# Kernel optimization log

Measured on AMD Instinct MI355X. Metric: run time of the kernel, lower is better.

The kernel has to match this reference:

```python
import jax, jax.numpy as jnp
import numpy as np

V, E, H, T = 50000, 1024, 1024, 128
L, MAXL = 50, 50
PAD, O_TOK = 0, 1


def setup_inputs() -> dict:
    key = jax.random.key(0)
    ks = jax.random.split(key, 18)
    s = 0.05
    f = lambda k, shape: jax.random.normal(k, shape, jnp.float32) * s
    return {
        'input_ids': jax.random.randint(ks[0], (1, L), 1, V),
        'tag_ids': jax.random.randint(ks[1], (1, L), 1, T),  # >=1 so no pad tags
        'word_embed': f(ks[2], (V, E)),
        'enc_Wih': f(ks[3], (3 * H, E)),
        'enc_Whh': f(ks[4], (3 * H, H)),
        'enc_bih': f(ks[5], (3 * H,)),
        'enc_bhh': f(ks[6], (3 * H,)),
        'dec_embed': f(ks[7], (T, H)),
        'attn_W': f(ks[8], (MAXL, 2 * H)),
        'attn_b': f(ks[9], (MAXL,)),
        'comb_W': f(ks[10], (H, 2 * H)),
        'comb_b': f(ks[11], (H,)),
        'dec_Wih': f(ks[12], (3 * H, H)),
        'dec_Whh': f(ks[13], (3 * H, H)),
        'dec_bih': f(ks[14], (3 * H,)),
        'dec_bhh': f(ks[15], (3 * H,)),
        'out_W': f(ks[16], (T, H)),
        'out_b': f(ks[17], (T,)),
    }


def _gru_cell(x, h, Wih, Whh, bih, bhh):
    # PyTorch GRU cell semantics
    gi = Wih @ x + bih
    gh = Whh @ h + bhh
    i_r, i_z, i_n = jnp.split(gi, 3)
    h_r, h_z, h_n = jnp.split(gh, 3)
    r = jax.nn.sigmoid(i_r + h_r)
    z = jax.nn.sigmoid(i_z + h_z)
    n = jnp.tanh(i_n + r * h_n)
    return (1.0 - z) * n + z * h


def _forward(word_embed, enc_Wih, enc_Whh, enc_bih, enc_bhh,
             dec_embed, attn_W, attn_b, comb_W, comb_b,
             dec_Wih, dec_Whh, dec_bih, dec_bhh, out_W, out_b,
             input_ids, tag_ids):
    src = input_ids[0]  # (L,)
    tgt = tag_ids[0]    # (L,)

    def enc_step(h, tok):
        h2 = _gru_cell(word_embed[tok], h, enc_Wih, enc_Whh, enc_bih, enc_bhh)
        return h2, h2

    h_enc, enc_outs = jax.lax.scan(enc_step, jnp.zeros((H,), word_embed.dtype), src)
    # enc_outs: (L, H); L == MAX_LENGTH so the buffer is fully filled

    dec_in = jnp.concatenate([jnp.array([O_TOK], tgt.dtype), tgt[:-1]])  # teacher forcing

    def dec_step(h, xt):
        tok, tgt_t = xt
        e = dec_embed[tok]  # (H,), dropout is identity in eval
        aw = jax.nn.softmax(attn_W @ jnp.concatenate([e, h]) + attn_b)  # (MAXL,)
        ctx = aw @ enc_outs  # (H,)
        o = jax.nn.relu(comb_W @ jnp.concatenate([e, ctx]) + comb_b)
        h2 = _gru_cell(o, h, dec_Wih, dec_Whh, dec_bih, dec_bhh)
        logp = jax.nn.log_softmax(out_W @ h2 + out_b)  # decoder output (log-probs)
        # original applies CrossEntropyLoss on log-probs -> log_softmax applied twice
        nll = -jax.nn.log_softmax(logp)[tgt_t]
        step_loss = jnp.where(tgt_t == PAD, jnp.zeros((), logp.dtype), nll)
        return h2, (logp, step_loss)

    _, (logps, losses) = jax.lax.scan(dec_step, h_enc, (dec_in, tgt))
    return logps, jnp.sum(losses)  # (L, T), scalar


def reference(input_ids, tag_ids, word_embed, enc_Wih, enc_Whh, enc_bih, enc_bhh,
              dec_embed, attn_W, attn_b, comb_W, comb_b,
              dec_Wih, dec_Whh, dec_bih, dec_bhh, out_W, out_b):
    return _forward(word_embed, enc_Wih, enc_Whh, enc_bih, enc_bhh,
                    dec_embed, attn_W, attn_b, comb_W, comb_b,
                    dec_Wih, dec_Whh, dec_bih, dec_bhh, out_W, out_b,
                    input_ids, tag_ids)
```

## Files before the change

### kernel.cpp

```cpp
#include <hip/hip_runtime.h>
#include <cstdint>


#define HDIM 1024
#define LSEQ 50
#define TDIM 128
#define G3   3072
#define PB   6
#define NPROD 128
#define LSTR 68

typedef float f32x4 __attribute__((ext_vector_type(4)));

struct KArgs {
  const int* input_ids; const int* tag_ids;
  const float* word_embed;
  const float* enc_Wih; const float* enc_Whh; const float* enc_bih; const float* enc_bhh;
  const float* dec_embed; const float* attn_W; const float* attn_b;
  const float* comb_W; const float* comb_b;
  const float* dec_Wih; const float* dec_Whh; const float* dec_bih; const float* dec_bhh;
  const float* out_W; const float* out_b;
  float* out;
  unsigned* ctrP; unsigned* ctrE; unsigned* ctrM; unsigned* ctrO; unsigned* ctrV;
  float* hbE;
  float* hbD;
  float* obD;
  float* awb;
  float* logits;
  float* GI;
  float* attn_e;
  float* pre_comb;
  float* MT;
  float* enc_outs;
};

__device__ __forceinline__ void fence_vm(){
  asm volatile("s_waitcnt vmcnt(0)" ::: "memory");
}
__device__ __forceinline__ void st_coh(float* p, float v){
  __hip_atomic_store(p, v, __ATOMIC_RELAXED, __HIP_MEMORY_SCOPE_AGENT);
}
__device__ __forceinline__ void st_tag(float* p, float v, unsigned tag){
  unsigned b = (__float_as_uint(v) & ~31u) | tag;
  st_coh(p, __uint_as_float(b));
}
__device__ __forceinline__ void stf(unsigned* p, unsigned v){
  __hip_atomic_store(p, v, __ATOMIC_RELAXED, __HIP_MEMORY_SCOPE_AGENT);
}
__device__ __forceinline__ unsigned ldu(const unsigned* p){
  return __hip_atomic_load(p, __ATOMIC_RELAXED, __HIP_MEMORY_SCOPE_AGENT);
}
__device__ __forceinline__ void addc(unsigned* base, int bid){
  __hip_atomic_fetch_add(base + (bid&7)*16, 1u, __ATOMIC_RELAXED, __HIP_MEMORY_SCOPE_AGENT);
}
__device__ __forceinline__ void addc0(unsigned* base){
  __hip_atomic_fetch_add(base, 1u, __ATOMIC_RELAXED, __HIP_MEMORY_SCOPE_AGENT);
}
__device__ __forceinline__ f32x4 coh_load4(const float* p){
  f32x4 v;
  asm volatile("global_load_dwordx4 %0, %1, off sc0 sc1\n\ts_waitcnt vmcnt(0)"
               : "=v"(v) : "v"(p) : "memory");
  return v;
}

template<int N>
__device__ __forceinline__ void wred_batch(float* v){
  #pragma unroll
  for(int o=32;o>0;o>>=1){
    #pragma unroll
    for(int i=0;i<N;i++) v[i] += __shfl_xor(v[i],o,64);
  }
}
__device__ __forceinline__ float wred_sum(float v){
  #pragma unroll
  for(int o=32;o>0;o>>=1) v += __shfl_xor(v,o,64);
  return v;
}
__device__ __forceinline__ float wred_max(float v){
  #pragma unroll
  for(int o=32;o>0;o>>=1) v = fmaxf(v,__shfl_xor(v,o,64));
  return v;
}

struct Chunk { f32x4 a,b,c,d; };
__device__ __forceinline__ Chunk load_chunk(const float* __restrict__ row, int lane){
  const f32x4* p = reinterpret_cast<const f32x4*>(row) + lane*4;
  Chunk w; w.a=p[0]; w.b=p[1]; w.c=p[2]; w.d=p[3]; return w;
}
__device__ __forceinline__ void pin(Chunk& c){
  asm volatile("" : "+v"(c.a), "+v"(c.b), "+v"(c.c), "+v"(c.d));
}
__device__ __forceinline__ void pinf(float& x){
  asm volatile("" : "+v"(x));
}
__device__ __forceinline__ float chunk_dot(const Chunk& w, const float* hc){
  return w.a.x*hc[0]+w.a.y*hc[1]+w.a.z*hc[2]+w.a.w*hc[3]
       + w.b.x*hc[4]+w.b.y*hc[5]+w.b.z*hc[6]+w.b.w*hc[7]
       + w.c.x*hc[8]+w.c.y*hc[9]+w.c.z*hc[10]+w.c.w*hc[11]
       + w.d.x*hc[12]+w.d.y*hc[13]+w.d.z*hc[14]+w.d.w*hc[15];
}
__device__ __forceinline__ void load_vec16(const float* __restrict__ v, float* hc, int lane){
  const f32x4* p = reinterpret_cast<const f32x4*>(v) + lane*4;
  f32x4 x0=p[0],x1=p[1],x2=p[2],x3=p[3];
  hc[0]=x0.x; hc[1]=x0.y; hc[2]=x0.z; hc[3]=x0.w;
  hc[4]=x1.x; hc[5]=x1.y; hc[6]=x1.z; hc[7]=x1.w;
  hc[8]=x2.x; hc[9]=x2.y; hc[10]=x2.z; hc[11]=x2.w;
  hc[12]=x3.x; hc[13]=x3.y; hc[14]=x3.z; hc[15]=x3.w;
}
__device__ __forceinline__ float sigm(float x){ return 1.f/(1.f+expf(-x)); }

template<int SLP>
__device__ __forceinline__ void stage_tag(float* ldsb, const float* g, int tid, unsigned tag){
  const float* p = g + 4*tid;
  f32x4 v;
  for(;;){
    v = coh_load4(p);
    unsigned m = ((__float_as_uint(v.x)&31u)^tag) | ((__float_as_uint(v.y)&31u)^tag)
               | ((__float_as_uint(v.z)&31u)^tag) | ((__float_as_uint(v.w)&31u)^tag);
    if(m==0u) break;
    if(SLP) __builtin_amdgcn_s_sleep(SLP);
  }
  int q = tid>>2, r4 = (tid&3)*4;
  ldsb[(r4+0)*LSTR+q]=v.x; ldsb[(r4+1)*LSTR+q]=v.y;
  ldsb[(r4+2)*LSTR+q]=v.z; ldsb[(r4+3)*LSTR+q]=v.w;
}
__device__ __forceinline__ void read16(const float* ldsb, float* hc, int lane){
  #pragma unroll
  for(int k=0;k<16;k++) hc[k]=ldsb[k*LSTR+lane];
}

__device__ __forceinline__ void wait8(const unsigned* base, unsigned n, int lane){
  const unsigned* p = base + lane*16;
  for(;;){
    unsigned v = (lane<8)? ldu(p) : 0xFFFFFFFFu;
    if(__all((int)(v>=n))) return;
    __builtin_amdgcn_s_sleep(8);
  }
}

__global__ __launch_bounds__(256,1) void seq2seq_kernel(KArgs A){
  const int bid = blockIdx.x, tid = threadIdx.x;
  const int wave = tid>>6, lane = tid&63;
  __shared__ float lds_h[16*LSTR+16];
  __shared__ float lds_o[16*LSTR+16];
  __shared__ float smr[64];
  __shared__ float smL[TDIM];
  __shared__ float smA[64];

  const int gv = bid*4 + wave;

  {
    const int r0 = gv*3;
    Chunk w0 = load_chunk(A.enc_Wih + (size_t)r0*HDIM, lane);
    Chunk w1 = load_chunk(A.enc_Wih + (size_t)(r0+1)*HDIM, lane);
    Chunk w2 = load_chunk(A.enc_Wih + (size_t)(r0+2)*HDIM, lane);
    float b0=A.enc_bih[r0], b1=A.enc_bih[r0+1], b2=A.enc_bih[r0+2];
    for(int te=0;te<LSEQ;++te){
      int tok = A.input_ids[te];
      float ec[16]; load_vec16(A.word_embed + (size_t)tok*HDIM, ec, lane);
      float d[3];
      d[0]=chunk_dot(w0,ec); d[1]=chunk_dot(w1,ec); d[2]=chunk_dot(w2,ec);
      wred_batch<3>(d);
      if(lane==0){
        st_coh(&A.GI[te*G3+r0],   d[0]+b0);
        st_coh(&A.GI[te*G3+r0+1], d[1]+b1);
        st_coh(&A.GI[te*G3+r0+2], d[2]+b2);
      }
    }
    Chunk wc = load_chunk(A.comb_W + (size_t)gv*2*HDIM, lane);
    float bc = A.comb_b[gv];
    Chunk wa; wa.a=0.f; wa.b=0.f; wa.c=0.f; wa.d=0.f;
    float ba = 0.f;
    if(gv < LSEQ){ wa = load_chunk(A.attn_W + (size_t)gv*2*HDIM, lane); ba = A.attn_b[gv]; }
    for(int t=0;t<LSEQ;++t){
      int tok = (t==0)?1:A.tag_ids[t-1];
      float ec[16]; load_vec16(A.dec_embed + (size_t)tok*HDIM, ec, lane);
      float d[2];
      d[0]=chunk_dot(wc,ec);
      d[1]=(gv<LSEQ)? chunk_dot(wa,ec) : 0.f;
      wred_batch<2>(d);
      if(lane==0){
        st_coh(&A.pre_comb[t*HDIM+gv], d[0]+bc);
        if(gv<LSEQ) st_coh(&A.attn_e[t*LSEQ+gv], d[1]+ba);
      }
    }
  }
  fence_vm();
  __syncthreads();
  if(tid==0) addc(A.ctrP, bid);
  if(wave==0) wait8(A.ctrP, 32u, lane);
  __syncthreads();

  const int p = bid - PB;
  const bool is_prod = (p>=0 && p<NPROD);
  const int base = is_prod ? p*8 : 0;
  const int j8 = base + (tid&7);

  if(is_prod){
    Chunk we[6];
    #pragma unroll
    for(int i=0;i<6;i++){
      int r = wave + 4*i;
      int le=r/3, g=r-3*le, row=g*HDIM+base+le;
      we[i] = load_chunk(A.enc_Whh + (size_t)row*HDIM, lane);
      pin(we[i]);
    }
    float bh0=A.enc_bhh[j8], bh1=A.enc_bhh[HDIM+j8], bh2=A.enc_bhh[2*HDIM+j8];
    for(int te=0;te<LSEQ;++te){
      const float* GIr = A.GI + te*G3;
      float gi0=GIr[j8], gi1=GIr[HDIM+j8], gi2=GIr[2*HDIM+j8];
      float hc[16];
      if(te>0){
        stage_tag<1>(lds_h, A.hbE + ((te-1)&1)*HDIM, tid, (unsigned)(te&31));
        __syncthreads();
        read16(lds_h, hc, lane);
      } else {
        for(int k=0;k<16;k++) hc[k]=0.f;
      }
      float part[6];
      #pragma unroll
      for(int i=0;i<6;i++) part[i]=chunk_dot(we[i],hc);
      wred_batch<6>(part);
      if(lane==0){
        #pragma unroll
        for(int i=0;i<6;i++) smr[wave+4*i]=part[i];
      }
      __syncthreads();
      if(tid<8){
        int j = base+tid;
        float gr=smr[tid*3]+bh0, gz=smr[tid*3+1]+bh1, gn=smr[tid*3+2]+bh2;
        float hj = (te>0)? lds_h[((j&15)*LSTR)+(j>>4)] : 0.f;
        float r_=sigm(gi0+gr), z_=sigm(gi1+gz);
        float n_=tanhf(gi2+r_*gn);
        float h2=(1.f-z_)*n_+z_*hj;
        st_tag(&A.hbE[(te&1)*HDIM+j], h2, (unsigned)((te+1)&31));
        st_coh(&A.enc_outs[te*HDIM+j], h2);
        if(te==LSEQ-1) st_tag(&A.hbD[j], h2, 0u);
      }
      __syncthreads();
    }
    fence_vm();
    __syncthreads();
    if(tid==0) addc(A.ctrE, bid);
  }
  if(wave==0) wait8(A.ctrE, 16u, lane);
  __syncthreads();

  {
    Chunk wm = load_chunk(A.comb_W + (size_t)gv*2*HDIM + HDIM, lane);
    for(int sg=0;sg<10;++sg){
      float pt[5];
      #pragma unroll
      for(int j=0;j<5;j++){
        float ec[16]; load_vec16(A.enc_outs + (sg*5+j)*HDIM, ec, lane);
        pt[j]=chunk_dot(wm,ec);
      }
      wred_batch<5>(pt);
      if(lane==0){
        #pragma unroll
        for(int j=0;j<5;j++) st_coh(&A.MT[(sg*5+j)*HDIM+gv], pt[j]);
      }
    }
  }
  fence_vm();
  __syncthreads();
  if(tid==0) addc(A.ctrM, bid);
  {
    const bool keep = is_prod || bid==0 || bid==4 ||
                      (bid>=134 && bid<154);
    if(!keep) return;
  }
  if(wave==0) wait8(A.ctrM, 32u, lane);
  __syncthreads();

  if(bid == 0){
    Chunk wa13[13];
    int srow[13];
    #pragma unroll
    for(int i=0;i<13;i++){
      int s = wave + 4*i; int sc = (s<LSEQ)? s : 0;
      wa13[i] = load_chunk(A.attn_W + (size_t)sc*2*HDIM + HDIM, lane);
      pin(wa13[i]);
      srow[i] = s;
    }
    for(int t=0;t<LSEQ;++t){
      float ae[13];
      #pragma unroll
      for(int i=0;i<13;i++)
        ae[i] = (srow[i]<LSEQ)? A.attn_e[t*LSEQ+srow[i]] : 0.f;
      stage_tag<1>(lds_h, A.hbD + (t%3)*HDIM, tid, (unsigned)(t&31));
      __syncthreads();
      float hc[16]; read16(lds_h, hc, lane);
      float pl[13];
      #pragma unroll
      for(int i=0;i<13;i++) pl[i]=chunk_dot(wa13[i],hc);
      wred_batch<13>(pl);
      if(lane==0){
        #pragma unroll
        for(int i=0;i<13;i++) if(srow[i]<LSEQ) smL[srow[i]]=pl[i]+ae[i];
      }
      __syncthreads();
      if(wave==0){
        float l = (lane<LSEQ)? smL[lane] : -1e30f;
        float m = wred_max(l);
        float pe = (lane<LSEQ)? expf(l-m) : 0.f;
        float ss = wred_sum(pe);
        float av = (lane<LSEQ)? pe/ss : 0.f;
        if(lane<52) st_tag(&A.awb[(t&1)*64+lane], av, (unsigned)(t&31));
      }
      __syncthreads();
    }
  } else if(bid>=150 && bid<154){
    const int i = (bid-150)*256 + tid;
    float m50[50];
    #pragma unroll
    for(int s=0;s<LSEQ;s++){ m50[s]=A.MT[s*HDIM+i]; pinf(m50[s]); }
    for(int t=0;t<LSEQ;++t){
      float pcv = A.pre_comb[t*HDIM+i];
      if(tid<13){
        const float* pp = A.awb + (t&1)*64 + 4*tid;
        const unsigned tg = (unsigned)(t&31);
        f32x4 v;
        for(;;){
          v = coh_load4(pp);
          unsigned m = ((__float_as_uint(v.x)&31u)^tg) | ((__float_as_uint(v.y)&31u)^tg)
                     | ((__float_as_uint(v.z)&31u)^tg) | ((__float_as_uint(v.w)&31u)^tg);
          if(m==0u) break;
        }
        smA[4*tid]=v.x; smA[4*tid+1]=v.y; smA[4*tid+2]=v.z; smA[4*tid+3]=v.w;
      }
      __syncthreads();
      float acc = pcv;
      #pragma unroll
      for(int s=0;s<LSEQ;s++) acc = fmaf(m50[s], smA[s], acc);
      st_tag(&A.obD[(t&1)*HDIM+i], fmaxf(acc,0.f), (unsigned)(t&31));
      __syncthreads();
    }
  } else if(bid == 4){
    float loss = 0.f;
    for(int t=0;t<LSEQ;++t){
      if(tid<32){
        const float* pp = A.logits + (t&1)*TDIM + 4*tid;
        const unsigned tg = (unsigned)(t&31);
        f32x4 v;
        for(;;){
          v = coh_load4(pp);
          unsigned m = ((__float_as_uint(v.x)&31u)^tg) | ((__float_as_uint(v.y)&31u)^tg)
                     | ((__float_as_uint(v.z)&31u)^tg) | ((__float_as_uint(v.w)&31u)^tg);
          if(m==0u) break;
          __builtin_amdgcn_s_sleep(1);
        }
        smL[4*tid]=v.x; smL[4*tid+1]=v.y; smL[4*tid+2]=v.z; smL[4*tid+3]=v.w;
      }
      __syncthreads();
      if(tid==0) stf(A.ctrV, (unsigned)(t+1));
      if(wave==0){
        float l0=smL[lane], l1=smL[lane+64];
        float m  = wred_max(fmaxf(l0,l1));
        float pe = expf(l0-m)+expf(l1-m);
        float s1 = wred_sum(pe);
        float lse = m + logf(s1);
        float lp0 = l0-lse, lp1 = l1-lse;
        float m2  = wred_max(fmaxf(lp0,lp1));
        float p2  = expf(lp0-m2)+expf(lp1-m2);
        float s2  = wred_sum(p2);
        float lse2 = m2 + logf(s2);
        A.out[t*TDIM + lane]      = lp0;
        A.out[t*TDIM + 64 + lane] = lp1;
        int tg2 = A.tag_ids[t];
        float c = ((lane==tg2)?(lse2-lp0):0.f) + ((lane+64==tg2)?(lse2-lp1):0.f);
        c = wred_sum(c);
        if(tg2 != 0) loss += c;
      }
      __syncthreads();
    }
    if(tid==0) A.out[LSEQ*TDIM] = loss;
  } else if(is_prod){
    Chunk wh[6], wi[6];
    #pragma unroll
    for(int i=0;i<6;i++){
      int r = wave + 4*i;
      int le=r/3, g=r-3*le, row=g*HDIM+base+le;
      wh[i] = load_chunk(A.dec_Whh + (size_t)row*HDIM, lane);
      pin(wh[i]);
      wi[i] = load_chunk(A.dec_Wih + (size_t)row*HDIM, lane);
      pin(wi[i]);
    }
    float dh0=A.dec_bhh[j8], dh1=A.dec_bhh[HDIM+j8], dh2=A.dec_bhh[2*HDIM+j8];
    float di0=A.dec_bih[j8], di1=A.dec_bih[HDIM+j8], di2=A.dec_bih[2*HDIM+j8];
    for(int t=0;t<LSEQ;++t){
      stage_tag<1>(lds_h, A.hbD + (t%3)*HDIM, tid, (unsigned)(t&31));
      __syncthreads();
      float hc[16]; read16(lds_h, hc, lane);
      float ph[6];
      #pragma unroll
      for(int i=0;i<6;i++) ph[i]=chunk_dot(wh[i],hc);
      wred_batch<6>(ph);
      if(lane==0){
        #pragma unroll
        for(int i=0;i<6;i++) smr[wave+4*i]=ph[i];
      }
      if(wave==0 && t>=3){
        const unsigned tgt = 16u*(unsigned)(t-2);
        for(;;){
          unsigned v = (lane==0)? ldu(A.ctrO) : tgt;
          if(__all((int)(v>=tgt))) break;
          __builtin_amdgcn_s_sleep(2);
        }
      }
      stage_tag<1>(lds_o, A.obD + (t&1)*HDIM, tid, (unsigned)(t&31));
      __syncthreads();
      float oc[16]; read16(lds_o, oc, lane);
      float po[6];
      #pragma unroll
      for(int i=0;i<6;i++) po[i]=chunk_dot(wi[i],oc);
      wred_batch<6>(po);
      if(lane==0){
        #pragma unroll
        for(int i=0;i<6;i++) smr[32+wave+4*i]=po[i];
      }
      __syncthreads();
      if(tid<8){
        int j = base+tid;
        float gr=smr[tid*3]+dh0,    gz=smr[tid*3+1]+dh1,    gn=smr[tid*3+2]+dh2;
        float ir=smr[32+tid*3]+di0, iz=smr[32+tid*3+1]+di1, inn=smr[32+tid*3+2]+di2;
        float hj = lds_h[((j&15)*LSTR)+(j>>4)];
        float r_=sigm(ir+gr), z_=sigm(iz+gz);
        float n_=tanhf(inn+r_*gn);
        float h2=(1.f-z_)*n_+z_*hj;
        st_tag(&A.hbD[((t+1)%3)*HDIM+j], h2, (unsigned)((t+1)&31));
      }
      __syncthreads();
    }
  } else {
    const int ob = bid-134;
    Chunk wo[2];
    float bo[2];
    #pragma unroll
    for(int i=0;i<2;i++){
      int row = ob*8 + wave*2 + i;
      wo[i]=load_chunk(A.out_W+(size_t)row*HDIM,lane);
      pin(wo[i]);
      bo[i]=A.out_b[row];
    }
    for(int t=0;t<LSEQ;++t){
      stage_tag<2>(lds_h, A.hbD + ((t+1)%3)*HDIM, tid, (unsigned)((t+1)&31));
      __syncthreads();
      if(tid==0) addc0(A.ctrO);
      float hc[16]; read16(lds_h, hc, lane);
      float pt[2]={chunk_dot(wo[0],hc),chunk_dot(wo[1],hc)};
      wred_batch<2>(pt);
      if(wave==0 && t>=2){
        const unsigned tgt = (unsigned)(t-1);
        for(;;){
          unsigned v = (lane==0)? ldu(A.ctrV) : tgt;
          if(__all((int)(v>=tgt))) break;
          __builtin_amdgcn_s_sleep(4);
        }
      }
      __syncthreads();
      if(lane==0){
        int row = ob*8 + wave*2;
        st_tag(&A.logits[(t&1)*TDIM + row],   pt[0]+bo[0], (unsigned)(t&31));
        st_tag(&A.logits[(t&1)*TDIM + row+1], pt[1]+bo[1], (unsigned)(t&31));
      }
      __syncthreads();
    }
  }
}

extern "C" void kernel_launch(void* const* d_in, const int* in_sizes, int n_in,
                              void* d_out, int out_size, void* d_ws, size_t ws_size,
                              hipStream_t stream){
  (void)in_sizes; (void)n_in; (void)out_size; (void)ws_size;
  KArgs A;
  A.input_ids = (const int*)d_in[0];
  A.tag_ids   = (const int*)d_in[1];
  A.word_embed= (const float*)d_in[2];
  A.enc_Wih   = (const float*)d_in[3];
  A.enc_Whh   = (const float*)d_in[4];
  A.enc_bih   = (const float*)d_in[5];
  A.enc_bhh   = (const float*)d_in[6];
  A.dec_embed = (const float*)d_in[7];
  A.attn_W    = (const float*)d_in[8];
  A.attn_b    = (const float*)d_in[9];
  A.comb_W    = (const float*)d_in[10];
  A.comb_b    = (const float*)d_in[11];
  A.dec_Wih   = (const float*)d_in[12];
  A.dec_Whh   = (const float*)d_in[13];
  A.dec_bih   = (const float*)d_in[14];
  A.dec_bhh   = (const float*)d_in[15];
  A.out_W     = (const float*)d_in[16];
  A.out_b     = (const float*)d_in[17];
  A.out       = (float*)d_out;

  unsigned* u = (unsigned*)d_ws;
  A.ctrP = u;
  A.ctrE = u + 128;
  A.ctrM = u + 256;
  A.ctrO = u + 384;
  A.ctrV = u + 448;
  float* f = (float*)d_ws + 1024;
  A.hbE    = f; f += 2*HDIM;
  A.hbD    = f; f += 3*HDIM;
  A.obD    = f; f += 2*HDIM;
  A.awb    = f; f += 2*64;
  A.logits = f; f += 2*TDIM;
  A.GI       = f; f += LSEQ*G3;
  A.attn_e   = f; f += LSEQ*LSEQ + 14;
  A.pre_comb = f; f += LSEQ*HDIM;
  A.MT       = f; f += LSEQ*HDIM;
  A.enc_outs = f; f += LSEQ*HDIM;

  (void)hipMemsetAsync(d_ws, 0, 4096, stream);
  (void)hipMemsetAsync((char*)d_ws + 4096, 0xFF, 7552*4, stream);
  void* args[] = { &A };
  hipError_t err = hipLaunchCooperativeKernel((const void*)seq2seq_kernel,
                                              dim3(256), dim3(256), args, 0, stream);
  if(err != hipSuccess){
    hipLaunchKernelGGL(seq2seq_kernel, dim3(256), dim3(256), 0, stream, A);
  }
}
```

Baseline: 561.2 us.

## Replace full-vector tag polling with sentinel-word polling plus fenced last-store

Each producer now writes its last element after a memory fence, so it acts as a sentinel. Consumers poll only those sentinel words with a single wave, then load the whole vector once without checking tags. Before, every thread spun on coherent 16-byte loads and checked a tag on every element, which put heavy polling traffic on the memory system. The new protocol adds an extra fence and barrier per step, and correctness now depends on the fence ordering the earlier stores before the sentinel. The weight pins are also moved inside the loops.

```diff
diff --git a/kernel.cpp b/kernel.cpp
--- a/kernel.cpp
+++ b/kernel.cpp
@@ -62,6 +62,43 @@
                : "=v"(v) : "v"(p) : "memory");
   return v;
 }
+__device__ __forceinline__ float coh_load1(const float* p){
+  float v;
+  asm volatile("global_load_dword %0, %1, off sc0 sc1\n\ts_waitcnt vmcnt(0)"
+               : "=v"(v) : "v"(p) : "memory");
+  return v;
+}
+
+__device__ __forceinline__ void wait_sent128(const float* g, unsigned tag, int lane){
+  const float* p0 = g + 8*lane + 7;
+  const float* p1 = g + 8*(lane+64) + 7;
+  for(;;){
+    float a,b;
+    asm volatile("global_load_dword %0, %2, off sc0 sc1\n\t"
+                 "global_load_dword %1, %3, off sc0 sc1\n\t"
+                 "s_waitcnt vmcnt(0)"
+                 : "=v"(a), "=v"(b) : "v"(p0), "v"(p1) : "memory");
+    unsigned m = ((__float_as_uint(a)&31u)^tag) | ((__float_as_uint(b)&31u)^tag);
+    if(__all((int)(m==0u))) return;
+    __builtin_amdgcn_s_sleep(2);
+  }
+}
+__device__ __forceinline__ void wait_sent4(const float* g, unsigned tag, int lane){
+  const float* p = g + ((lane&3)<<8) + 255;
+  for(;;){
+    float a = coh_load1(p);
+    bool ok = (lane<4)? ((__float_as_uint(a)&31u)==tag) : true;
+    if(__all((int)ok)) return;
+    __builtin_amdgcn_s_sleep(1);
+  }
+}
+__device__ __forceinline__ void wait_sent1(const float* p, unsigned tag){
+  for(;;){
+    float a = coh_load1(p);
+    if((__float_as_uint(a)&31u)==tag) return;
+    __builtin_amdgcn_s_sleep(1);
+  }
+}
 
 template<int N>
 __device__ __forceinline__ void wred_batch(float* v){
@@ -109,17 +146,8 @@
 }
 __device__ __forceinline__ float sigm(float x){ return 1.f/(1.f+expf(-x)); }
 
-template<int SLP>
-__device__ __forceinline__ void stage_tag(float* ldsb, const float* g, int tid, unsigned tag){
-  const float* p = g + 4*tid;
-  f32x4 v;
-  for(;;){
-    v = coh_load4(p);
-    unsigned m = ((__float_as_uint(v.x)&31u)^tag) | ((__float_as_uint(v.y)&31u)^tag)
-               | ((__float_as_uint(v.z)&31u)^tag) | ((__float_as_uint(v.w)&31u)^tag);
-    if(m==0u) break;
-    if(SLP) __builtin_amdgcn_s_sleep(SLP);
-  }
+__device__ __forceinline__ void stage_fast(float* ldsb, const float* g, int tid){
+  f32x4 v = coh_load4(g + 4*tid);
   int q = tid>>2, r4 = (tid&3)*4;
   ldsb[(r4+0)*LSTR+q]=v.x; ldsb[(r4+1)*LSTR+q]=v.y;
   ldsb[(r4+2)*LSTR+q]=v.z; ldsb[(r4+3)*LSTR+q]=v.w;
@@ -203,15 +231,18 @@
       int r = wave + 4*i;
       int le=r/3, g=r-3*le, row=g*HDIM+base+le;
       we[i] = load_chunk(A.enc_Whh + (size_t)row*HDIM, lane);
-      pin(we[i]);
     }
     float bh0=A.enc_bhh[j8], bh1=A.enc_bhh[HDIM+j8], bh2=A.enc_bhh[2*HDIM+j8];
     for(int te=0;te<LSEQ;++te){
+      #pragma unroll
+      for(int i=0;i<6;i++) pin(we[i]);
       const float* GIr = A.GI + te*G3;
       float gi0=GIr[j8], gi1=GIr[HDIM+j8], gi2=GIr[2*HDIM+j8];
       float hc[16];
       if(te>0){
-        stage_tag<1>(lds_h, A.hbE + ((te-1)&1)*HDIM, tid, (unsigned)(te&31));
+        if(wave==0) wait_sent128(A.hbE + ((te-1)&1)*HDIM, (unsigned)(te&31), lane);
+        __syncthreads();
+        stage_fast(lds_h, A.hbE + ((te-1)&1)*HDIM, tid);
         __syncthreads();
         read16(lds_h, hc, lane);
       } else {
@@ -226,15 +257,23 @@
         for(int i=0;i<6;i++) smr[wave+4*i]=part[i];
       }
       __syncthreads();
+      float h2=0.f; int j=0;
       if(tid<8){
-        int j = base+tid;
+        j = base+tid;
         float gr=smr[tid*3]+bh0, gz=smr[tid*3+1]+bh1, gn=smr[tid*3+2]+bh2;
         float hj = (te>0)? lds_h[((j&15)*LSTR)+(j>>4)] : 0.f;
         float r_=sigm(gi0+gr), z_=sigm(gi1+gz);
         float n_=tanhf(gi2+r_*gn);
-        float h2=(1.f-z_)*n_+z_*hj;
+        h2=(1.f-z_)*n_+z_*hj;
+        st_coh(&A.enc_outs[te*HDIM+j], h2);
+        if(tid<7){
+          st_tag(&A.hbE[(te&1)*HDIM+j], h2, (unsigned)((te+1)&31));
+          if(te==LSEQ-1) st_tag(&A.hbD[j], h2, 0u);
+        }
+      }
+      fence_vm();
+      if(tid==7){
         st_tag(&A.hbE[(te&1)*HDIM+j], h2, (unsigned)((te+1)&31));
-        st_coh(&A.enc_outs[te*HDIM+j], h2);
         if(te==LSEQ-1) st_tag(&A.hbD[j], h2, 0u);
       }
       __syncthreads();
@@ -280,15 +319,19 @@
     for(int i=0;i<13;i++){
       int s = wave + 4*i; int sc = (s<LSEQ)? s : 0;
       wa13[i] = load_chunk(A.attn_W + (size_t)sc*2*HDIM + HDIM, lane);
-      pin(wa13[i]);
       srow[i] = s;
     }
     for(int t=0;t<LSEQ;++t){
+      #pragma unroll
+      for(int i=0;i<13;i++) pin(wa13[i]);
+      const unsigned tg = (unsigned)(t&31);
       float ae[13];
       #pragma unroll
       for(int i=0;i<13;i++)
         ae[i] = (srow[i]<LSEQ)? A.attn_e[t*LSEQ+srow[i]] : 0.f;
-      stage_tag<1>(lds_h, A.hbD + (t%3)*HDIM, tid, (unsigned)(t&31));
+      if(wave==0) wait_sent128(A.hbD + (t%3)*HDIM, tg, lane);
+      __syncthreads();
+      stage_fast(lds_h, A.hbD + (t%3)*HDIM, tid);
       __syncthreads();
       float hc[16]; read16(lds_h, hc, lane);
       float pl[13];
@@ -300,40 +343,44 @@
         for(int i=0;i<13;i++) if(srow[i]<LSEQ) smL[srow[i]]=pl[i]+ae[i];
       }
       __syncthreads();
+      float av=0.f;
       if(wave==0){
         float l = (lane<LSEQ)? smL[lane] : -1e30f;
         float m = wred_max(l);
         float pe = (lane<LSEQ)? expf(l-m) : 0.f;
         float ss = wred_sum(pe);
-        float av = (lane<LSEQ)? pe/ss : 0.f;
-        if(lane<52) st_tag(&A.awb[(t&1)*64+lane], av, (unsigned)(t&31));
-      }
+        av = (lane<LSEQ)? pe/ss : 0.f;
+        if(lane<51) st_tag(&A.awb[(t&1)*64+lane], av, tg);
+      }
+      fence_vm();
+      if(wave==0 && lane==51) st_tag(&A.awb[(t&1)*64+51], av, tg);
       __syncthreads();
     }
   } else if(bid>=150 && bid<154){
     const int i = (bid-150)*256 + tid;
     float m50[50];
     #pragma unroll
-    for(int s=0;s<LSEQ;s++){ m50[s]=A.MT[s*HDIM+i]; pinf(m50[s]); }
+    for(int s=0;s<LSEQ;s++) m50[s]=A.MT[s*HDIM+i];
     for(int t=0;t<LSEQ;++t){
+      #pragma unroll
+      for(int s=0;s<LSEQ;s++) pinf(m50[s]);
+      const unsigned tg = (unsigned)(t&31);
       float pcv = A.pre_comb[t*HDIM+i];
+      if(wave==0) wait_sent1(A.awb + (t&1)*64 + 51, tg);
+      __syncthreads();
       if(tid<13){
-        const float* pp = A.awb + (t&1)*64 + 4*tid;
-        const unsigned tg = (unsigned)(t&31);
-        f32x4 v;
-        for(;;){
-          v = coh_load4(pp);
-          unsigned m = ((__float_as_uint(v.x)&31u)^tg) | ((__float_as_uint(v.y)&31u)^tg)
-                     | ((__float_as_uint(v.z)&31u)^tg) | ((__float_as_uint(v.w)&31u)^tg);
-          if(m==0u) break;
-        }
+        f32x4 v = coh_load4(A.awb + (t&1)*64 + 4*tid);
         smA[4*tid]=v.x; smA[4*tid+1]=v.y; smA[4*tid+2]=v.z; smA[4*tid+3]=v.w;
       }
       __syncthreads();
       float acc = pcv;
       #pragma unroll
       for(int s=0;s<LSEQ;s++) acc = fmaf(m50[s], smA[s], acc);
-      st_tag(&A.obD[(t&1)*HDIM+i], fmaxf(acc,0.f), (unsigned)(t&31));
+      float ov = fmaxf(acc,0.f);
+      if(tid<255) st_tag(&A.obD[(t&1)*HDIM+i], ov, tg);
+      fence_vm();
+      __syncthreads();
+      if(tid==255) st_tag(&A.obD[(t&1)*HDIM+i], ov, tg);
       __syncthreads();
     }
   } else if(bid == 4){
@@ -348,7 +395,7 @@
           unsigned m = ((__float_as_uint(v.x)&31u)^tg) | ((__float_as_uint(v.y)&31u)^tg)
                      | ((__float_as_uint(v.z)&31u)^tg) | ((__float_as_uint(v.w)&31u)^tg);
           if(m==0u) break;
-          __builtin_amdgcn_s_sleep(1);
+          __builtin_amdgcn_s_sleep(2);
         }
         smL[4*tid]=v.x; smL[4*tid+1]=v.y; smL[4*tid+2]=v.z; smL[4*tid+3]=v.w;
       }
@@ -382,14 +429,17 @@
       int r = wave + 4*i;
       int le=r/3, g=r-3*le, row=g*HDIM+base+le;
       wh[i] = load_chunk(A.dec_Whh + (size_t)row*HDIM, lane);
-      pin(wh[i]);
       wi[i] = load_chunk(A.dec_Wih + (size_t)row*HDIM, lane);
-      pin(wi[i]);
     }
     float dh0=A.dec_bhh[j8], dh1=A.dec_bhh[HDIM+j8], dh2=A.dec_bhh[2*HDIM+j8];
     float di0=A.dec_bih[j8], di1=A.dec_bih[HDIM+j8], di2=A.dec_bih[2*HDIM+j8];
     for(int t=0;t<LSEQ;++t){
-      stage_tag<1>(lds_h, A.hbD + (t%3)*HDIM, tid, (unsigned)(t&31));
+      #pragma unroll
+      for(int i=0;i<6;i++){ pin(wh[i]); pin(wi[i]); }
+      const unsigned tg = (unsigned)(t&31);
+      if(wave==0) wait_sent128(A.hbD + (t%3)*HDIM, tg, lane);
+      __syncthreads();
+      stage_fast(lds_h, A.hbD + (t%3)*HDIM, tid);
       __syncthreads();
       float hc[16]; read16(lds_h, hc, lane);
       float ph[6];
@@ -408,7 +458,9 @@
           __builtin_amdgcn_s_sleep(2);
         }
       }
-      stage_tag<1>(lds_o, A.obD + (t&1)*HDIM, tid, (unsigned)(t&31));
+      if(wave==0) wait_sent4(A.obD + (t&1)*HDIM, tg, lane);
+      __syncthreads();
+      stage_fast(lds_o, A.obD + (t&1)*HDIM, tid);
       __syncthreads();
       float oc[16]; read16(lds_o, oc, lane);
       float po[6];
@@ -420,16 +472,19 @@
         for(int i=0;i<6;i++) smr[32+wave+4*i]=po[i];
       }
       __syncthreads();
+      float h2=0.f; int j=0;
       if(tid<8){
-        int j = base+tid;
+        j = base+tid;
         float gr=smr[tid*3]+dh0,    gz=smr[tid*3+1]+dh1,    gn=smr[tid*3+2]+dh2;
         float ir=smr[32+tid*3]+di0, iz=smr[32+tid*3+1]+di1, inn=smr[32+tid*3+2]+di2;
         float hj = lds_h[((j&15)*LSTR)+(j>>4)];
         float r_=sigm(ir+gr), z_=sigm(iz+gz);
         float n_=tanhf(inn+r_*gn);
-        float h2=(1.f-z_)*n_+z_*hj;
-        st_tag(&A.hbD[((t+1)%3)*HDIM+j], h2, (unsigned)((t+1)&31));
-      }
+        h2=(1.f-z_)*n_+z_*hj;
+        if(tid<7) st_tag(&A.hbD[((t+1)%3)*HDIM+j], h2, (unsigned)((t+1)&31));
+      }
+      fence_vm();
+      if(tid==7) st_tag(&A.hbD[((t+1)%3)*HDIM+j], h2, (unsigned)((t+1)&31));
       __syncthreads();
     }
   } else {
@@ -440,11 +495,14 @@
     for(int i=0;i<2;i++){
       int row = ob*8 + wave*2 + i;
       wo[i]=load_chunk(A.out_W+(size_t)row*HDIM,lane);
-      pin(wo[i]);
       bo[i]=A.out_b[row];
     }
     for(int t=0;t<LSEQ;++t){
-      stage_tag<2>(lds_h, A.hbD + ((t+1)%3)*HDIM, tid, (unsigned)((t+1)&31));
+      pin(wo[0]); pin(wo[1]);
+      const unsigned tg1 = (unsigned)((t+1)&31);
+      if(wave==0) wait_sent128(A.hbD + ((t+1)%3)*HDIM, tg1, lane);
+      __syncthreads();
+      stage_fast(lds_h, A.hbD + ((t+1)%3)*HDIM, tid);
       __syncthreads();
       if(tid==0) addc0(A.ctrO);
       float hc[16]; read16(lds_h, hc, lane);
```

Measured after the change: 660.8 us. +17.7%, slower.

## Pack recurrent weights to fp16 with fdot2 and fuse attention-combine blocks

Applied to the files above, without the earlier changes.

Weights held in registers for the encoder and decoder GRU, attention and output projections are converted to packed fp16, and dot products use v_dot2 (fdot2) against fp16-staged hidden vectors in LDS. The attention-softmax block and the separate combine blocks are merged into four blocks that each compute the softmax locally and apply it to packed MT columns. This drops the awb global handoff and one cross-block wait per step. It also halves register and LDS footprint and the FMA count. The cost is reduced precision on recurrent state over 50 steps, plus redundant attention computation across four blocks.

```diff
diff --git a/kernel.cpp b/kernel.cpp
--- a/kernel.cpp
+++ b/kernel.cpp
@@ -8,9 +8,19 @@
 #define G3   3072
 #define PB   6
 #define NPROD 128
-#define LSTR 68
+#define LSTRP 65
 
 typedef float f32x4 __attribute__((ext_vector_type(4)));
+typedef _Float16 h2 __attribute__((ext_vector_type(2)));
+
+#if __has_builtin(__builtin_amdgcn_fdot2)
+#define FDOT2(a,b,c) __builtin_amdgcn_fdot2((a),(b),(c),false)
+#else
+__device__ __forceinline__ float fdot2_sw(h2 a, h2 b, float c){
+  return c + (float)a[0]*(float)b[0] + (float)a[1]*(float)b[1];
+}
+#define FDOT2(a,b,c) fdot2_sw((a),(b),(c))
+#endif
 
 struct KArgs {
   const int* input_ids; const int* tag_ids;
@@ -25,7 +35,6 @@
   float* hbE;
   float* hbD;
   float* obD;
-  float* awb;
   float* logits;
   float* GI;
   float* attn_e;
@@ -87,12 +96,6 @@
   const f32x4* p = reinterpret_cast<const f32x4*>(row) + lane*4;
   Chunk w; w.a=p[0]; w.b=p[1]; w.c=p[2]; w.d=p[3]; return w;
 }
-__device__ __forceinline__ void pin(Chunk& c){
-  asm volatile("" : "+v"(c.a), "+v"(c.b), "+v"(c.c), "+v"(c.d));
-}
-__device__ __forceinline__ void pinf(float& x){
-  asm volatile("" : "+v"(x));
-}
 __device__ __forceinline__ float chunk_dot(const Chunk& w, const float* hc){
   return w.a.x*hc[0]+w.a.y*hc[1]+w.a.z*hc[2]+w.a.w*hc[3]
        + w.b.x*hc[4]+w.b.y*hc[5]+w.b.z*hc[6]+w.b.w*hc[7]
@@ -107,10 +110,38 @@
   hc[8]=x2.x; hc[9]=x2.y; hc[10]=x2.z; hc[11]=x2.w;
   hc[12]=x3.x; hc[13]=x3.y; hc[14]=x3.z; hc[15]=x3.w;
 }
+
+struct PChunk { unsigned m[8]; };
+__device__ __forceinline__ h2 as_h2(unsigned u){ return __builtin_bit_cast(h2, u); }
+__device__ __forceinline__ unsigned as_u(h2 h){ return __builtin_bit_cast(unsigned, h); }
+__device__ __forceinline__ unsigned pack2(float a, float b){
+  return as_u((h2){(_Float16)a, (_Float16)b});
+}
+__device__ __forceinline__ PChunk load_pchunk(const float* __restrict__ row, int lane){
+  const f32x4* p = reinterpret_cast<const f32x4*>(row) + lane*4;
+  f32x4 a=p[0],b=p[1],c=p[2],d=p[3];
+  PChunk w;
+  w.m[0]=pack2(a.x,a.y); w.m[1]=pack2(a.z,a.w);
+  w.m[2]=pack2(b.x,b.y); w.m[3]=pack2(b.z,b.w);
+  w.m[4]=pack2(c.x,c.y); w.m[5]=pack2(c.z,c.w);
+  w.m[6]=pack2(d.x,d.y); w.m[7]=pack2(d.z,d.w);
+  return w;
+}
+__device__ __forceinline__ void pinp(PChunk& c){
+  asm volatile("" : "+v"(c.m[0]),"+v"(c.m[1]),"+v"(c.m[2]),"+v"(c.m[3]),
+                    "+v"(c.m[4]),"+v"(c.m[5]),"+v"(c.m[6]),"+v"(c.m[7]));
+}
+__device__ __forceinline__ void pin32(unsigned& x){ asm volatile("" : "+v"(x)); }
+__device__ __forceinline__ float pdot(const PChunk& w, const h2* hp){
+  float acc = 0.f;
+  #pragma unroll
+  for(int k=0;k<8;k++) acc = FDOT2(as_h2(w.m[k]), hp[k], acc);
+  return acc;
+}
 __device__ __forceinline__ float sigm(float x){ return 1.f/(1.f+expf(-x)); }
 
 template<int SLP>
-__device__ __forceinline__ void stage_tag(float* ldsb, const float* g, int tid, unsigned tag){
+__device__ __forceinline__ void stage_tag_p(h2* ldsp, const float* g, int tid, unsigned tag){
   const float* p = g + 4*tid;
   f32x4 v;
   for(;;){
@@ -120,13 +151,18 @@
     if(m==0u) break;
     if(SLP) __builtin_amdgcn_s_sleep(SLP);
   }
-  int q = tid>>2, r4 = (tid&3)*4;
-  ldsb[(r4+0)*LSTR+q]=v.x; ldsb[(r4+1)*LSTR+q]=v.y;
-  ldsb[(r4+2)*LSTR+q]=v.z; ldsb[(r4+3)*LSTR+q]=v.w;
-}
-__device__ __forceinline__ void read16(const float* ldsb, float* hc, int lane){
+  int q = tid>>2, m0 = (tid&3)*2;
+  ldsp[m0*LSTRP+q]     = (h2){(_Float16)v.x,(_Float16)v.y};
+  ldsp[(m0+1)*LSTRP+q] = (h2){(_Float16)v.z,(_Float16)v.w};
+}
+__device__ __forceinline__ void read8p(const h2* ldsp, h2* hp, int lane){
   #pragma unroll
-  for(int k=0;k<16;k++) hc[k]=ldsb[k*LSTR+lane];
+  for(int k=0;k<8;k++) hp[k]=ldsp[k*LSTRP+lane];
+}
+__device__ __forceinline__ float hread(const h2* ldsp, int j){
+  int pj = j>>1;
+  h2 v = ldsp[(pj&7)*LSTRP + (pj>>3)];
+  return (float)v[j&1];
 }
 
 __device__ __forceinline__ void wait8(const unsigned* base, unsigned n, int lane){
@@ -141,8 +177,9 @@
 __global__ __launch_bounds__(256,1) void seq2seq_kernel(KArgs A){
   const int bid = blockIdx.x, tid = threadIdx.x;
   const int wave = tid>>6, lane = tid&63;
-  __shared__ float lds_h[16*LSTR+16];
-  __shared__ float lds_o[16*LSTR+16];
+  __shared__ h2 ldsp_h[8*LSTRP+8];
+  __shared__ h2 ldsp_o[8*LSTRP+8];
+  __shared__ h2 awpL[32];
   __shared__ float smr[64];
   __shared__ float smL[TDIM];
   __shared__ float smA[64];
@@ -197,29 +234,30 @@
   const int j8 = base + (tid&7);
 
   if(is_prod){
-    Chunk we[6];
+    PChunk wep[6];
     #pragma unroll
     for(int i=0;i<6;i++){
       int r = wave + 4*i;
       int le=r/3, g=r-3*le, row=g*HDIM+base+le;
-      we[i] = load_chunk(A.enc_Whh + (size_t)row*HDIM, lane);
-      pin(we[i]);
+      wep[i] = load_pchunk(A.enc_Whh + (size_t)row*HDIM, lane);
+      pinp(wep[i]);
     }
     float bh0=A.enc_bhh[j8], bh1=A.enc_bhh[HDIM+j8], bh2=A.enc_bhh[2*HDIM+j8];
     for(int te=0;te<LSEQ;++te){
       const float* GIr = A.GI + te*G3;
       float gi0=GIr[j8], gi1=GIr[HDIM+j8], gi2=GIr[2*HDIM+j8];
-      float hc[16];
+      h2 hp[8];
       if(te>0){
-        stage_tag<1>(lds_h, A.hbE + ((te-1)&1)*HDIM, tid, (unsigned)(te&31));
+        stage_tag_p<1>(ldsp_h, A.hbE + ((te-1)&1)*HDIM, tid, (unsigned)(te&31));
         __syncthreads();
-        read16(lds_h, hc, lane);
+        read8p(ldsp_h, hp, lane);
       } else {
-        for(int k=0;k<16;k++) hc[k]=0.f;
+        #pragma unroll
+        for(int k=0;k<8;k++) hp[k]=(h2){(_Float16)0.f,(_Float16)0.f};
       }
       float part[6];
       #pragma unroll
-      for(int i=0;i<6;i++) part[i]=chunk_dot(we[i],hc);
+      for(int i=0;i<6;i++) part[i]=pdot(wep[i],hp);
       wred_batch<6>(part);
       if(lane==0){
         #pragma unroll
@@ -229,13 +267,13 @@
       if(tid<8){
         int j = base+tid;
         float gr=smr[tid*3]+bh0, gz=smr[tid*3+1]+bh1, gn=smr[tid*3+2]+bh2;
-        float hj = (te>0)? lds_h[((j&15)*LSTR)+(j>>4)] : 0.f;
+        float hj = (te>0)? hread(ldsp_h, j) : 0.f;
         float r_=sigm(gi0+gr), z_=sigm(gi1+gz);
         float n_=tanhf(gi2+r_*gn);
-        float h2=(1.f-z_)*n_+z_*hj;
-        st_tag(&A.hbE[(te&1)*HDIM+j], h2, (unsigned)((te+1)&31));
-        st_coh(&A.enc_outs[te*HDIM+j], h2);
-        if(te==LSEQ-1) st_tag(&A.hbD[j], h2, 0u);
+        float h2v=(1.f-z_)*n_+z_*hj;
+        st_tag(&A.hbE[(te&1)*HDIM+j], h2v, (unsigned)((te+1)&31));
+        st_coh(&A.enc_outs[te*HDIM+j], h2v);
+        if(te==LSEQ-1) st_tag(&A.hbD[j], h2v, 0u);
       }
       __syncthreads();
     }
@@ -266,34 +304,42 @@
   __syncthreads();
   if(tid==0) addc(A.ctrM, bid);
   {
-    const bool keep = is_prod || bid==0 || bid==4 ||
-                      (bid>=134 && bid<154);
+    const bool keep = is_prod || bid<5 || (bid>=134 && bid<150);
     if(!keep) return;
   }
   if(wave==0) wait8(A.ctrM, 32u, lane);
   __syncthreads();
 
-  if(bid == 0){
-    Chunk wa13[13];
+  if(bid < 4){
+    const int oi = bid*256 + tid;
+    PChunk wa13[13];
     int srow[13];
     #pragma unroll
     for(int i=0;i<13;i++){
       int s = wave + 4*i; int sc = (s<LSEQ)? s : 0;
-      wa13[i] = load_chunk(A.attn_W + (size_t)sc*2*HDIM + HDIM, lane);
-      pin(wa13[i]);
+      wa13[i] = load_pchunk(A.attn_W + (size_t)sc*2*HDIM + HDIM, lane);
+      pinp(wa13[i]);
       srow[i] = s;
     }
+    unsigned mp[25];
+    #pragma unroll
+    for(int k=0;k<25;k++){
+      mp[k] = pack2(A.MT[(2*k)*HDIM+oi], A.MT[(2*k+1)*HDIM+oi]);
+      pin32(mp[k]);
+    }
     for(int t=0;t<LSEQ;++t){
+      const unsigned tg = (unsigned)(t&31);
       float ae[13];
       #pragma unroll
       for(int i=0;i<13;i++)
         ae[i] = (srow[i]<LSEQ)? A.attn_e[t*LSEQ+srow[i]] : 0.f;
-      stage_tag<1>(lds_h, A.hbD + (t%3)*HDIM, tid, (unsigned)(t&31));
-      __syncthreads();
-      float hc[16]; read16(lds_h, hc, lane);
+      float pcv = A.pre_comb[t*HDIM+oi];
+      stage_tag_p<1>(ldsp_h, A.hbD + (t%3)*HDIM, tid, tg);
+      __syncthreads();
+      h2 hp[8]; read8p(ldsp_h, hp, lane);
       float pl[13];
       #pragma unroll
-      for(int i=0;i<13;i++) pl[i]=chunk_dot(wa13[i],hc);
+      for(int i=0;i<13;i++) pl[i]=pdot(wa13[i],hp);
       wred_batch<13>(pl);
       if(lane==0){
         #pragma unroll
@@ -305,35 +351,15 @@
         float m = wred_max(l);
         float pe = (lane<LSEQ)? expf(l-m) : 0.f;
         float ss = wred_sum(pe);
-        float av = (lane<LSEQ)? pe/ss : 0.f;
-        if(lane<52) st_tag(&A.awb[(t&1)*64+lane], av, (unsigned)(t&31));
-      }
-      __syncthreads();
-    }
-  } else if(bid>=150 && bid<154){
-    const int i = (bid-150)*256 + tid;
-    float m50[50];
-    #pragma unroll
-    for(int s=0;s<LSEQ;s++){ m50[s]=A.MT[s*HDIM+i]; pinf(m50[s]); }
-    for(int t=0;t<LSEQ;++t){
-      float pcv = A.pre_comb[t*HDIM+i];
-      if(tid<13){
-        const float* pp = A.awb + (t&1)*64 + 4*tid;
-        const unsigned tg = (unsigned)(t&31);
-        f32x4 v;
-        for(;;){
-          v = coh_load4(pp);
-          unsigned m = ((__float_as_uint(v.x)&31u)^tg) | ((__float_as_uint(v.y)&31u)^tg)
-                     | ((__float_as_uint(v.z)&31u)^tg) | ((__float_as_uint(v.w)&31u)^tg);
-          if(m==0u) break;
-        }
-        smA[4*tid]=v.x; smA[4*tid+1]=v.y; smA[4*tid+2]=v.z; smA[4*tid+3]=v.w;
-      }
+        if(lane<LSEQ) smA[lane] = pe/ss;
+      }
+      __syncthreads();
+      if(tid<25) awpL[tid] = (h2){(_Float16)smA[2*tid],(_Float16)smA[2*tid+1]};
       __syncthreads();
       float acc = pcv;
       #pragma unroll
-      for(int s=0;s<LSEQ;s++) acc = fmaf(m50[s], smA[s], acc);
-      st_tag(&A.obD[(t&1)*HDIM+i], fmaxf(acc,0.f), (unsigned)(t&31));
+      for(int k=0;k<25;k++) acc = FDOT2(as_h2(mp[k]), awpL[k], acc);
+      st_tag(&A.obD[(t&1)*HDIM+oi], fmaxf(acc,0.f), tg);
       __syncthreads();
     }
   } else if(bid == 4){
@@ -348,7 +374,7 @@
           unsigned m = ((__float_as_uint(v.x)&31u)^tg) | ((__float_as_uint(v.y)&31u)^tg)
                      | ((__float_as_uint(v.z)&31u)^tg) | ((__float_as_uint(v.w)&31u)^tg);
           if(m==0u) break;
-          __builtin_amdgcn_s_sleep(1);
+          __builtin_amdgcn_s_sleep(2);
         }
         smL[4*tid]=v.x; smL[4*tid+1]=v.y; smL[4*tid+2]=v.z; smL[4*tid+3]=v.w;
       }
@@ -376,25 +402,26 @@
     }
     if(tid==0) A.out[LSEQ*TDIM] = loss;
   } else if(is_prod){
-    Chunk wh[6], wi[6];
+    PChunk whp[6], wip[6];
     #pragma unroll
     for(int i=0;i<6;i++){
       int r = wave + 4*i;
       int le=r/3, g=r-3*le, row=g*HDIM+base+le;
-      wh[i] = load_chunk(A.dec_Whh + (size_t)row*HDIM, lane);
-      pin(wh[i]);
-      wi[i] = load_chunk(A.dec_Wih + (size_t)row*HDIM, lane);
-      pin(wi[i]);
+      whp[i] = load_pchunk(A.dec_Whh + (size_t)row*HDIM, lane);
+      pinp(whp[i]);
+      wip[i] = load_pchunk(A.dec_Wih + (size_t)row*HDIM, lane);
+      pinp(wip[i]);
     }
     float dh0=A.dec_bhh[j8], dh1=A.dec_bhh[HDIM+j8], dh2=A.dec_bhh[2*HDIM+j8];
     float di0=A.dec_bih[j8], di1=A.dec_bih[HDIM+j8], di2=A.dec_bih[2*HDIM+j8];
     for(int t=0;t<LSEQ;++t){
-      stage_tag<1>(lds_h, A.hbD + (t%3)*HDIM, tid, (unsigned)(t&31));
-      __syncthreads();
-      float hc[16]; read16(lds_h, hc, lane);
+      const unsigned tg = (unsigned)(t&31);
+      stage_tag_p<1>(ldsp_h, A.hbD + (t%3)*HDIM, tid, tg);
+      __syncthreads();
+      h2 hp[8]; read8p(ldsp_h, hp, lane);
       float ph[6];
       #pragma unroll
-      for(int i=0;i<6;i++) ph[i]=chunk_dot(wh[i],hc);
+      for(int i=0;i<6;i++) ph[i]=pdot(whp[i],hp);
       wred_batch<6>(ph);
       if(lane==0){
         #pragma unroll
@@ -408,12 +435,12 @@
           __builtin_amdgcn_s_sleep(2);
         }
       }
-      stage_tag<1>(lds_o, A.obD + (t&1)*HDIM, tid, (unsigned)(t&31));
-      __syncthreads();
-      float oc[16]; read16(lds_o, oc, lane);
+      stage_tag_p<1>(ldsp_o, A.obD + (t&1)*HDIM, tid, tg);
+      __syncthreads();
+      h2 op[8]; read8p(ldsp_o, op, lane);
       float po[6];
       #pragma unroll
-      for(int i=0;i<6;i++) po[i]=chunk_dot(wi[i],oc);
+      for(int i=0;i<6;i++) po[i]=pdot(wip[i],op);
       wred_batch<6>(po);
       if(lane==0){
         #pragma unroll
@@ -424,31 +451,32 @@
         int j = base+tid;
         float gr=smr[tid*3]+dh0,    gz=smr[tid*3+1]+dh1,    gn=smr[tid*3+2]+dh2;
         float ir=smr[32+tid*3]+di0, iz=smr[32+tid*3+1]+di1, inn=smr[32+tid*3+2]+di2;
-        float hj = lds_h[((j&15)*LSTR)+(j>>4)];
+        float hj = hread(ldsp_h, j);
         float r_=sigm(ir+gr), z_=sigm(iz+gz);
         float n_=tanhf(inn+r_*gn);
-        float h2=(1.f-z_)*n_+z_*hj;
-        st_tag(&A.hbD[((t+1)%3)*HDIM+j], h2, (unsigned)((t+1)&31));
+        float h2v=(1.f-z_)*n_+z_*hj;
+        st_tag(&A.hbD[((t+1)%3)*HDIM+j], h2v, (unsigned)((t+1)&31));
       }
       __syncthreads();
     }
   } else {
     const int ob = bid-134;
-    Chunk wo[2];
+    PChunk wop[2];
     float bo[2];
     #pragma unroll
     for(int i=0;i<2;i++){
       int row = ob*8 + wave*2 + i;
-      wo[i]=load_chunk(A.out_W+(size_t)row*HDIM,lane);
-      pin(wo[i]);
+      wop[i]=load_pchunk(A.out_W+(size_t)row*HDIM,lane);
+      pinp(wop[i]);
       bo[i]=A.out_b[row];
     }
     for(int t=0;t<LSEQ;++t){
-      stage_tag<2>(lds_h, A.hbD + ((t+1)%3)*HDIM, tid, (unsigned)((t+1)&31));
+      const unsigned tg1 = (unsigned)((t+1)&31);
+      stage_tag_p<2>(ldsp_h, A.hbD + ((t+1)%3)*HDIM, tid, tg1);
       __syncthreads();
       if(tid==0) addc0(A.ctrO);
-      float hc[16]; read16(lds_h, hc, lane);
-      float pt[2]={chunk_dot(wo[0],hc),chunk_dot(wo[1],hc)};
+      h2 hp[8]; read8p(ldsp_h, hp, lane);
+      float pt[2]={pdot(wop[0],hp),pdot(wop[1],hp)};
       wred_batch<2>(pt);
       if(wave==0 && t>=2){
         const unsigned tgt = (unsigned)(t-1);
@@ -504,7 +532,6 @@
   A.hbE    = f; f += 2*HDIM;
   A.hbD    = f; f += 3*HDIM;
   A.obD    = f; f += 2*HDIM;
-  A.awb    = f; f += 2*64;
   A.logits = f; f += 2*TDIM;
   A.GI       = f; f += LSEQ*G3;
   A.attn_e   = f; f += LSEQ*LSEQ + 14;
@@ -513,7 +540,7 @@
   A.enc_outs = f; f += LSEQ*HDIM;
 
   (void)hipMemsetAsync(d_ws, 0, 4096, stream);
-  (void)hipMemsetAsync((char*)d_ws + 4096, 0xFF, 7552*4, stream);
+  (void)hipMemsetAsync((char*)d_ws + 4096, 0xFF, 7424*4, stream);
   void* args[] = { &A };
   hipError_t err = hipLaunchCooperativeKernel((const void*)seq2seq_kernel,
                                               dim3(256), dim3(256), args, 0, stream);
```

Result: faster. 511.2 us (-8.9%).
